# Performance work log

Measured on AMD Instinct MI355X. Metric: run time of the kernel, lower is better.

The kernel has to match this reference:

```python
import jax, jax.numpy as jnp
import numpy as np

N_HEADS = 16

def setup_inputs() -> dict:
    key = jax.random.key(0)
    k1, k2 = jax.random.split(key)
    qkv = jax.random.normal(k1, (4, 3072, 2048), dtype=jnp.float32)
    encoder_kv = jax.random.normal(k2, (4, 2048, 256), dtype=jnp.float32)
    return {"qkv": qkv, "encoder_kv": encoder_kv}

def reference(qkv, encoder_kv):
    bs, width, length = qkv.shape
    ch = width // (3 * N_HEADS)  # 64
    # [bs*H, 3*ch, T] -> q, k, v each [bs*H, ch, T]
    q, k, v = jnp.split(qkv.reshape(bs * N_HEADS, 3 * ch, length), 3, axis=1)
    # encoder kv: [bs, H*2*ch, S] -> ek, ev each [bs*H, ch, S]
    ek, ev = jnp.split(encoder_kv.reshape(bs * N_HEADS, 2 * ch, -1), 2, axis=1)
    k = jnp.concatenate([ek, k], axis=-1)  # [bs*H, ch, S+T]
    v = jnp.concatenate([ev, v], axis=-1)
    scale = ch ** -0.25  # 1/sqrt(sqrt(ch)), applied to both q and k
    weight = jnp.einsum('bct,bcs->bts', q * scale, k * scale)  # [bs*H, T, S+T]
    weight = jax.nn.softmax(weight.astype(jnp.float32), axis=-1).astype(qkv.dtype)
    a = jnp.einsum('bts,bcs->bct', weight, v)  # [bs*H, ch, T]
    return a.reshape(bs, -1, length)
```

## Files before the change

kernel.cpp:

```cpp
#include <hip/hip_runtime.h>
#include <hip/hip_bf16.h>

typedef __attribute__((ext_vector_type(8))) short bf16x8;
typedef __attribute__((ext_vector_type(4))) float f32x4;
typedef __attribute__((ext_vector_type(4))) unsigned u32x4;
typedef __attribute__((ext_vector_type(2))) unsigned u32x2;

#define T_LEN 2048
#define S_ENC 256
#define QSCALE 0.18033688011112042f

#define BARRIER() __syncthreads()

__device__ __forceinline__ float exp2_hw(float x) {
#if __has_builtin(__builtin_amdgcn_exp2f)
  return __builtin_amdgcn_exp2f(x);
#else
  float r;
  asm("v_exp_f32 %0, %1" : "=v"(r) : "v"(x));
  return r;
#endif
}

__device__ __forceinline__ unsigned cvt_pk_bf16(float lo, float hi) {
  unsigned r;
  asm("v_cvt_pk_bf16_f32 %0, %1, %2" : "=v"(r) : "v"(lo), "v"(hi));
  return r;
}

__device__ __forceinline__ short f2bf(float x) {
  union { __hip_bfloat16 b; short s; } u;
  u.b = __float2bfloat16(x);
  return u.s;
}

__device__ __forceinline__ int swz(int row, int col) {
  return row * 64 + (col ^ ((row & 7) << 3));
}

union PU { u32x4 u; bf16x8 b; };

template<int STRIDE>
__device__ __forceinline__ void issue_loads(
    const float* __restrict__ kb, const float* __restrict__ vb, int s0, int tid,
    float (&kr)[8], float (&kr2)[8], f32x4 (&vr)[4]) {
  const int ks = tid & 63;
  const int kc = (tid >> 6) * 8;
  const float* kp = kb + (size_t)kc * STRIDE + (s0 + ks);
  const float* kp2 = kp + (size_t)32 * STRIDE;
#pragma unroll
  for (int r = 0; r < 8; ++r) kr[r] = kp[(size_t)r * STRIDE];
#pragma unroll
  for (int r = 0; r < 8; ++r) kr2[r] = kp2[(size_t)r * STRIDE];
  const int vg = tid & 15;
  const int vc = tid >> 4;
  const float* vp0 = vb + (size_t)vc * STRIDE + (s0 + 4 * vg);
  vr[0] = *(const f32x4*)(vp0);
  vr[1] = *(const f32x4*)(vp0 + (size_t)32 * STRIDE);
  vr[2] = *(const f32x4*)(vp0 + (size_t)16 * STRIDE);
  vr[3] = *(const f32x4*)(vp0 + (size_t)48 * STRIDE);
}

__device__ __forceinline__ void stage_write(
    short* __restrict__ Kt, short* __restrict__ Vt, int tid,
    const float (&kr)[8], const float (&kr2)[8], const f32x4 (&vr)[4]) {
  const int ks = tid & 63;
  const int kc = (tid >> 6) * 8;
  u32x4 kw;
#pragma unroll
  for (int r = 0; r < 4; ++r) kw[r] = cvt_pk_bf16(kr[2 * r], kr[2 * r + 1]);
  *(u32x4*)(Kt + swz(ks, kc)) = kw;
  u32x4 kw2;
#pragma unroll
  for (int r = 0; r < 4; ++r) kw2[r] = cvt_pk_bf16(kr2[2 * r], kr2[2 * r + 1]);
  *(u32x4*)(Kt + swz(ks, kc + 32)) = kw2;

  const int vg = tid & 15;
  const int vc = tid >> 4;
  const int vcol = 32 * (vg >> 3) + 8 * (vg & 3) + 4 * ((vg >> 2) & 1);
  const int vrow[4] = {vc, vc + 32, vc + 16, vc + 48};
#pragma unroll
  for (int i = 0; i < 4; ++i) {
    u32x2 vw;
    vw[0] = cvt_pk_bf16(vr[i][0], vr[i][1]);
    vw[1] = cvt_pk_bf16(vr[i][2], vr[i][3]);
    *(u32x2*)(Vt + swz(vrow[i], vcol)) = vw;
  }
}

__device__ __forceinline__ void compute_tile(
    const short* __restrict__ Kt, const short* __restrict__ Vt,
    const bf16x8 (&qf)[4][2], f32x4 (&o)[4][4], float (&lp)[4], int tid) {
  const int lane = tid & 63;
  const int ln = lane & 15;
  const int lg = lane >> 4;

  bf16x8 kf[4][2];
#pragma unroll
  for (int mt = 0; mt < 4; ++mt) {
    const int row = 16 * mt + ln;
    kf[mt][0] = *(const bf16x8*)(Kt + swz(row, 8 * lg));
    kf[mt][1] = *(const bf16x8*)(Kt + swz(row, 32 + 8 * lg));
  }

  PU pfrag[4][2];
#pragma unroll
  for (int pr = 0; pr < 2; ++pr) {
    f32x4 sacc[2][4];
#pragma unroll
    for (int q2 = 0; q2 < 2; ++q2)
#pragma unroll
      for (int mt = 0; mt < 4; ++mt) sacc[q2][mt] = (f32x4){0.f, 0.f, 0.f, 0.f};

#pragma unroll
    for (int mt = 0; mt < 4; ++mt)
#pragma unroll
      for (int q2 = 0; q2 < 2; ++q2) {
        const int qt = 2 * pr + q2;
        sacc[q2][mt] = __builtin_amdgcn_mfma_f32_16x16x32_bf16(kf[mt][0], qf[qt][0], sacc[q2][mt], 0, 0, 0);
        sacc[q2][mt] = __builtin_amdgcn_mfma_f32_16x16x32_bf16(kf[mt][1], qf[qt][1], sacc[q2][mt], 0, 0, 0);
      }

#pragma unroll
    for (int q2 = 0; q2 < 2; ++q2) {
      const int qt = 2 * pr + q2;
      float pmt[4];
#pragma unroll
      for (int mt = 0; mt < 4; ++mt) {
        float p0 = exp2_hw(sacc[q2][mt][0]);
        float p1 = exp2_hw(sacc[q2][mt][1]);
        float p2 = exp2_hw(sacc[q2][mt][2]);
        float p3 = exp2_hw(sacc[q2][mt][3]);
        pfrag[qt][mt >> 1].u[2 * (mt & 1) + 0] = cvt_pk_bf16(p0, p1);
        pfrag[qt][mt >> 1].u[2 * (mt & 1) + 1] = cvt_pk_bf16(p2, p3);
        pmt[mt] = (p0 + p1) + (p2 + p3);
      }
      lp[qt] += (pmt[0] + pmt[1]) + (pmt[2] + pmt[3]);
    }
  }

#pragma unroll
  for (int sub = 0; sub < 2; ++sub)
#pragma unroll
    for (int ct = 0; ct < 4; ++ct) {
      const bf16x8 vf = *(const bf16x8*)(Vt + swz(16 * ct + ln, 32 * sub + 8 * lg));
#pragma unroll
      for (int qt = 0; qt < 4; ++qt)
        o[qt][ct] = __builtin_amdgcn_mfma_f32_16x16x32_bf16(vf, pfrag[qt][sub].b, o[qt][ct], 0, 0, 0);
    }
}

__global__ __launch_bounds__(256, 2) void attn_kernel(
    const float* __restrict__ qkv, const float* __restrict__ ekv,
    float* __restrict__ out) {
  const int tid = threadIdx.x;
  const int lane = tid & 63;
  const int wave = tid >> 6;
  const int ln = lane & 15;
  const int lg = lane >> 4;

  const int bh = blockIdx.x & 63;
  const int qb = blockIdx.x >> 6;
  const int t0 = qb * 256 + wave * 64;

  const float* qp  = qkv + (size_t)bh * 192 * T_LEN;
  const float* kp  = qp + (size_t)64 * T_LEN;
  const float* vp  = qp + (size_t)128 * T_LEN;
  const float* ekp = ekv + (size_t)bh * 128 * S_ENC;
  const float* evp = ekp + (size_t)64 * S_ENC;

  __shared__ __attribute__((aligned(16))) short Kt[2][64 * 64];
  __shared__ __attribute__((aligned(16))) short Vt[2][64 * 64];

  bf16x8 qf[4][2];
#pragma unroll
  for (int qt = 0; qt < 4; ++qt)
#pragma unroll
    for (int kk = 0; kk < 2; ++kk)
#pragma unroll
      for (int j = 0; j < 8; ++j)
        qf[qt][kk][j] =
            f2bf(qp[(size_t)(32 * kk + 8 * lg + j) * T_LEN + (t0 + 16 * qt + ln)] * QSCALE);

  f32x4 o[4][4];
#pragma unroll
  for (int qt = 0; qt < 4; ++qt)
#pragma unroll
    for (int ct = 0; ct < 4; ++ct) o[qt][ct] = (f32x4){0.f, 0.f, 0.f, 0.f};
  float lp[4] = {0.f, 0.f, 0.f, 0.f};

  for (int st = 0; st < 4; ++st) {
    float kr[8], kr2[8];
    f32x4 vr[4];
    issue_loads<S_ENC>(ekp, evp, 64 * st, tid, kr, kr2, vr);
    BARRIER();
    stage_write(&Kt[0][0], &Vt[0][0], tid, kr, kr2, vr);
    BARRIER();
    compute_tile(&Kt[0][0], &Vt[0][0], qf, o, lp, tid);
  }

  {
    float kr[8], kr2[8];
    f32x4 vr[4];
    issue_loads<T_LEN>(kp, vp, 0, tid, kr, kr2, vr);
    BARRIER();
    stage_write(&Kt[0][0], &Vt[0][0], tid, kr, kr2, vr);
    issue_loads<T_LEN>(kp, vp, 64, tid, kr, kr2, vr);
    BARRIER();

    int cur = 0;
#pragma unroll 1
    for (int t = 0; t < 31; ++t) {
      stage_write(&Kt[cur ^ 1][0], &Vt[cur ^ 1][0], tid, kr, kr2, vr);
      if (t < 30)
        issue_loads<T_LEN>(kp, vp, 64 * (t + 2), tid, kr, kr2, vr);
      compute_tile(&Kt[cur][0], &Vt[cur][0], qf, o, lp, tid);
      BARRIER();
      cur ^= 1;
    }
    compute_tile(&Kt[cur][0], &Vt[cur][0], qf, o, lp, tid);
  }

#pragma unroll
  for (int qt = 0; qt < 4; ++qt) {
    float l = lp[qt];
    l += __shfl_xor(l, 16);
    l += __shfl_xor(l, 32);
    const float inv = 1.0f / l;
    float* ob = out + (size_t)bh * 64 * T_LEN + (t0 + 16 * qt + ln);
#pragma unroll
    for (int ct = 0; ct < 4; ++ct)
#pragma unroll
      for (int r = 0; r < 4; ++r)
        ob[(size_t)(16 * ct + 4 * lg + r) * T_LEN] = o[qt][ct][r] * inv;
  }
}

extern "C" void kernel_launch(void* const* d_in, const int* in_sizes, int n_in,
                              void* d_out, int out_size, void* d_ws, size_t ws_size,
                              hipStream_t stream) {
  const float* qkv = (const float*)d_in[0];
  const float* ekv = (const float*)d_in[1];
  float* out = (float*)d_out;
  attn_kernel<<<dim3(512), dim3(256), 0, stream>>>(qkv, ekv, out);
}
```

Before: 98.77 us.

## Interleave softmax exp with PV MFMAs and drop LDS double buffering

```diff
diff --git a/kernel.cpp b/kernel.cpp
--- a/kernel.cpp
+++ b/kernel.cpp
@@ -9,7 +9,6 @@
 #define T_LEN 2048
 #define S_ENC 256
 #define QSCALE 0.18033688011112042f
-
 #define BARRIER() __syncthreads()
 
 __device__ __forceinline__ float exp2_hw(float x) {
@@ -88,6 +87,22 @@
   }
 }
 
+__device__ __forceinline__ void softmax_qt(const f32x4 (&sa)[4], PU (&pf)[2],
+                                           float& lpq) {
+  float pmt[4];
+#pragma unroll
+  for (int mt = 0; mt < 4; ++mt) {
+    float p0 = exp2_hw(sa[mt][0]);
+    float p1 = exp2_hw(sa[mt][1]);
+    float p2 = exp2_hw(sa[mt][2]);
+    float p3 = exp2_hw(sa[mt][3]);
+    pf[mt >> 1].u[2 * (mt & 1) + 0] = cvt_pk_bf16(p0, p1);
+    pf[mt >> 1].u[2 * (mt & 1) + 1] = cvt_pk_bf16(p2, p3);
+    pmt[mt] = (p0 + p1) + (p2 + p3);
+  }
+  lpq += (pmt[0] + pmt[1]) + (pmt[2] + pmt[3]);
+}
+
 __device__ __forceinline__ void compute_tile(
     const short* __restrict__ Kt, const short* __restrict__ Vt,
     const bf16x8 (&qf)[4][2], f32x4 (&o)[4][4], float (&lp)[4], int tid) {
@@ -103,50 +118,59 @@
     kf[mt][1] = *(const bf16x8*)(Kt + swz(row, 32 + 8 * lg));
   }
 
-  PU pfrag[4][2];
-#pragma unroll
-  for (int pr = 0; pr < 2; ++pr) {
-    f32x4 sacc[2][4];
-#pragma unroll
-    for (int q2 = 0; q2 < 2; ++q2)
-#pragma unroll
-      for (int mt = 0; mt < 4; ++mt) sacc[q2][mt] = (f32x4){0.f, 0.f, 0.f, 0.f};
-
-#pragma unroll
-    for (int mt = 0; mt < 4; ++mt)
-#pragma unroll
-      for (int q2 = 0; q2 < 2; ++q2) {
-        const int qt = 2 * pr + q2;
-        sacc[q2][mt] = __builtin_amdgcn_mfma_f32_16x16x32_bf16(kf[mt][0], qf[qt][0], sacc[q2][mt], 0, 0, 0);
-        sacc[q2][mt] = __builtin_amdgcn_mfma_f32_16x16x32_bf16(kf[mt][1], qf[qt][1], sacc[q2][mt], 0, 0, 0);
-      }
-
+  f32x4 sa[2][4];
+#pragma unroll
+  for (int q2 = 0; q2 < 2; ++q2)
+#pragma unroll
+    for (int mt = 0; mt < 4; ++mt) sa[q2][mt] = (f32x4){0.f, 0.f, 0.f, 0.f};
+#pragma unroll
+  for (int mt = 0; mt < 4; ++mt)
 #pragma unroll
     for (int q2 = 0; q2 < 2; ++q2) {
-      const int qt = 2 * pr + q2;
-      float pmt[4];
-#pragma unroll
-      for (int mt = 0; mt < 4; ++mt) {
-        float p0 = exp2_hw(sacc[q2][mt][0]);
-        float p1 = exp2_hw(sacc[q2][mt][1]);
-        float p2 = exp2_hw(sacc[q2][mt][2]);
-        float p3 = exp2_hw(sacc[q2][mt][3]);
-        pfrag[qt][mt >> 1].u[2 * (mt & 1) + 0] = cvt_pk_bf16(p0, p1);
-        pfrag[qt][mt >> 1].u[2 * (mt & 1) + 1] = cvt_pk_bf16(p2, p3);
-        pmt[mt] = (p0 + p1) + (p2 + p3);
-      }
-      lp[qt] += (pmt[0] + pmt[1]) + (pmt[2] + pmt[3]);
+      sa[q2][mt] = __builtin_amdgcn_mfma_f32_16x16x32_bf16(kf[mt][0], qf[q2][0], sa[q2][mt], 0, 0, 0);
+      sa[q2][mt] = __builtin_amdgcn_mfma_f32_16x16x32_bf16(kf[mt][1], qf[q2][1], sa[q2][mt], 0, 0, 0);
     }
-  }
+
+  PU pf0[2][2];
+  softmax_qt(sa[0], pf0[0], lp[0]);
+  softmax_qt(sa[1], pf0[1], lp[1]);
+
+#pragma unroll
+  for (int q2 = 0; q2 < 2; ++q2)
+#pragma unroll
+    for (int mt = 0; mt < 4; ++mt) sa[q2][mt] = (f32x4){0.f, 0.f, 0.f, 0.f};
+#pragma unroll
+  for (int mt = 0; mt < 4; ++mt)
+#pragma unroll
+    for (int q2 = 0; q2 < 2; ++q2) {
+      sa[q2][mt] = __builtin_amdgcn_mfma_f32_16x16x32_bf16(kf[mt][0], qf[2 + q2][0], sa[q2][mt], 0, 0, 0);
+      sa[q2][mt] = __builtin_amdgcn_mfma_f32_16x16x32_bf16(kf[mt][1], qf[2 + q2][1], sa[q2][mt], 0, 0, 0);
+    }
+
+  bf16x8 vf[2][4];
+  PU pf1[2][2];
+#pragma unroll
+  for (int ct = 0; ct < 4; ++ct) {
+    vf[0][ct] = *(const bf16x8*)(Vt + swz(16 * ct + ln, 8 * lg));
+    o[0][ct] = __builtin_amdgcn_mfma_f32_16x16x32_bf16(vf[0][ct], pf0[0][0].b, o[0][ct], 0, 0, 0);
+    o[1][ct] = __builtin_amdgcn_mfma_f32_16x16x32_bf16(vf[0][ct], pf0[1][0].b, o[1][ct], 0, 0, 0);
+  }
+  softmax_qt(sa[0], pf1[0], lp[2]);
+
+#pragma unroll
+  for (int ct = 0; ct < 4; ++ct) {
+    vf[1][ct] = *(const bf16x8*)(Vt + swz(16 * ct + ln, 32 + 8 * lg));
+    o[0][ct] = __builtin_amdgcn_mfma_f32_16x16x32_bf16(vf[1][ct], pf0[0][1].b, o[0][ct], 0, 0, 0);
+    o[1][ct] = __builtin_amdgcn_mfma_f32_16x16x32_bf16(vf[1][ct], pf0[1][1].b, o[1][ct], 0, 0, 0);
+  }
+  softmax_qt(sa[1], pf1[1], lp[3]);
 
 #pragma unroll
   for (int sub = 0; sub < 2; ++sub)
 #pragma unroll
     for (int ct = 0; ct < 4; ++ct) {
-      const bf16x8 vf = *(const bf16x8*)(Vt + swz(16 * ct + ln, 32 * sub + 8 * lg));
-#pragma unroll
-      for (int qt = 0; qt < 4; ++qt)
-        o[qt][ct] = __builtin_amdgcn_mfma_f32_16x16x32_bf16(vf, pfrag[qt][sub].b, o[qt][ct], 0, 0, 0);
+      o[2][ct] = __builtin_amdgcn_mfma_f32_16x16x32_bf16(vf[sub][ct], pf1[0][sub].b, o[2][ct], 0, 0, 0);
+      o[3][ct] = __builtin_amdgcn_mfma_f32_16x16x32_bf16(vf[sub][ct], pf1[1][sub].b, o[3][ct], 0, 0, 0);
     }
 }
 
@@ -169,8 +193,8 @@
   const float* ekp = ekv + (size_t)bh * 128 * S_ENC;
   const float* evp = ekp + (size_t)64 * S_ENC;
 
-  __shared__ __attribute__((aligned(16))) short Kt[2][64 * 64];
-  __shared__ __attribute__((aligned(16))) short Vt[2][64 * 64];
+  __shared__ __attribute__((aligned(16))) short Kt[64 * 64];
+  __shared__ __attribute__((aligned(16))) short Vt[64 * 64];
 
   bf16x8 qf[4][2];
 #pragma unroll
@@ -194,31 +218,18 @@
     f32x4 vr[4];
     issue_loads<S_ENC>(ekp, evp, 64 * st, tid, kr, kr2, vr);
     BARRIER();
-    stage_write(&Kt[0][0], &Vt[0][0], tid, kr, kr2, vr);
-    BARRIER();
-    compute_tile(&Kt[0][0], &Vt[0][0], qf, o, lp, tid);
-  }
-
-  {
+    stage_write(Kt, Vt, tid, kr, kr2, vr);
+    BARRIER();
+    compute_tile(Kt, Vt, qf, o, lp, tid);
+  }
+  for (int st = 0; st < 32; ++st) {
     float kr[8], kr2[8];
     f32x4 vr[4];
-    issue_loads<T_LEN>(kp, vp, 0, tid, kr, kr2, vr);
-    BARRIER();
-    stage_write(&Kt[0][0], &Vt[0][0], tid, kr, kr2, vr);
-    issue_loads<T_LEN>(kp, vp, 64, tid, kr, kr2, vr);
-    BARRIER();
-
-    int cur = 0;
-#pragma unroll 1
-    for (int t = 0; t < 31; ++t) {
-      stage_write(&Kt[cur ^ 1][0], &Vt[cur ^ 1][0], tid, kr, kr2, vr);
-      if (t < 30)
-        issue_loads<T_LEN>(kp, vp, 64 * (t + 2), tid, kr, kr2, vr);
-      compute_tile(&Kt[cur][0], &Vt[cur][0], qf, o, lp, tid);
-      BARRIER();
-      cur ^= 1;
-    }
-    compute_tile(&Kt[cur][0], &Vt[cur][0], qf, o, lp, tid);
+    issue_loads<T_LEN>(kp, vp, 64 * st, tid, kr, kr2, vr);
+    BARRIER();
+    stage_write(Kt, Vt, tid, kr, kr2, vr);
+    BARRIER();
+    compute_tile(Kt, Vt, qf, o, lp, tid);
   }
 
 #pragma unroll
```

After: 91.78 us. 1.08x faster.

## Load V fragments directly from global memory and drop K double buffering

Applied to the files above, without the earlier changes.

```diff
diff --git a/kernel.cpp b/kernel.cpp
--- a/kernel.cpp
+++ b/kernel.cpp
@@ -4,12 +4,10 @@
 typedef __attribute__((ext_vector_type(8))) short bf16x8;
 typedef __attribute__((ext_vector_type(4))) float f32x4;
 typedef __attribute__((ext_vector_type(4))) unsigned u32x4;
-typedef __attribute__((ext_vector_type(2))) unsigned u32x2;
 
 #define T_LEN 2048
 #define S_ENC 256
 #define QSCALE 0.18033688011112042f
-
 #define BARRIER() __syncthreads()
 
 __device__ __forceinline__ float exp2_hw(float x) {
@@ -42,8 +40,8 @@
 
 template<int STRIDE>
 __device__ __forceinline__ void issue_loads(
-    const float* __restrict__ kb, const float* __restrict__ vb, int s0, int tid,
-    float (&kr)[8], float (&kr2)[8], f32x4 (&vr)[4]) {
+    const float* __restrict__ kb, int s0, int tid,
+    float (&kr)[8], float (&kr2)[8]) {
   const int ks = tid & 63;
   const int kc = (tid >> 6) * 8;
   const float* kp = kb + (size_t)kc * STRIDE + (s0 + ks);
@@ -52,18 +50,11 @@
   for (int r = 0; r < 8; ++r) kr[r] = kp[(size_t)r * STRIDE];
 #pragma unroll
   for (int r = 0; r < 8; ++r) kr2[r] = kp2[(size_t)r * STRIDE];
-  const int vg = tid & 15;
-  const int vc = tid >> 4;
-  const float* vp0 = vb + (size_t)vc * STRIDE + (s0 + 4 * vg);
-  vr[0] = *(const f32x4*)(vp0);
-  vr[1] = *(const f32x4*)(vp0 + (size_t)32 * STRIDE);
-  vr[2] = *(const f32x4*)(vp0 + (size_t)16 * STRIDE);
-  vr[3] = *(const f32x4*)(vp0 + (size_t)48 * STRIDE);
 }
 
 __device__ __forceinline__ void stage_write(
-    short* __restrict__ Kt, short* __restrict__ Vt, int tid,
-    const float (&kr)[8], const float (&kr2)[8], const f32x4 (&vr)[4]) {
+    short* __restrict__ Kt, int tid,
+    const float (&kr)[8], const float (&kr2)[8]) {
   const int ks = tid & 63;
   const int kc = (tid >> 6) * 8;
   u32x4 kw;
@@ -74,26 +65,23 @@
 #pragma unroll
   for (int r = 0; r < 4; ++r) kw2[r] = cvt_pk_bf16(kr2[2 * r], kr2[2 * r + 1]);
   *(u32x4*)(Kt + swz(ks, kc + 32)) = kw2;
-
-  const int vg = tid & 15;
-  const int vc = tid >> 4;
-  const int vcol = 32 * (vg >> 3) + 8 * (vg & 3) + 4 * ((vg >> 2) & 1);
-  const int vrow[4] = {vc, vc + 32, vc + 16, vc + 48};
-#pragma unroll
-  for (int i = 0; i < 4; ++i) {
-    u32x2 vw;
-    vw[0] = cvt_pk_bf16(vr[i][0], vr[i][1]);
-    vw[1] = cvt_pk_bf16(vr[i][2], vr[i][3]);
-    *(u32x2*)(Vt + swz(vrow[i], vcol)) = vw;
-  }
-}
-
+}
+
+template<int STRIDE>
 __device__ __forceinline__ void compute_tile(
-    const short* __restrict__ Kt, const short* __restrict__ Vt,
+    const short* __restrict__ Kt, const float* __restrict__ vt ,
     const bf16x8 (&qf)[4][2], f32x4 (&o)[4][4], float (&lp)[4], int tid) {
   const int lane = tid & 63;
   const int ln = lane & 15;
   const int lg = lane >> 4;
+
+  f32x4 va[4], vb_[4], vc_[4], vd[4];
+#pragma unroll
+  for (int ct = 0; ct < 4; ++ct) {
+    const float* p = vt + (size_t)(16 * ct + ln) * STRIDE + 4 * lg;
+    va[ct] = *(const f32x4*)p;
+    vb_[ct] = *(const f32x4*)(p + 16);
+  }
 
   bf16x8 kf[4][2];
 #pragma unroll
@@ -120,6 +108,15 @@
         sacc[q2][mt] = __builtin_amdgcn_mfma_f32_16x16x32_bf16(kf[mt][0], qf[qt][0], sacc[q2][mt], 0, 0, 0);
         sacc[q2][mt] = __builtin_amdgcn_mfma_f32_16x16x32_bf16(kf[mt][1], qf[qt][1], sacc[q2][mt], 0, 0, 0);
       }
+
+    if (pr == 0) {
+#pragma unroll
+      for (int ct = 0; ct < 4; ++ct) {
+        const float* p = vt + (size_t)(16 * ct + ln) * STRIDE + 32 + 4 * lg;
+        vc_[ct] = *(const f32x4*)p;
+        vd[ct] = *(const f32x4*)(p + 16);
+      }
+    }
 
 #pragma unroll
     for (int q2 = 0; q2 < 2; ++q2) {
@@ -143,10 +140,16 @@
   for (int sub = 0; sub < 2; ++sub)
 #pragma unroll
     for (int ct = 0; ct < 4; ++ct) {
-      const bf16x8 vf = *(const bf16x8*)(Vt + swz(16 * ct + ln, 32 * sub + 8 * lg));
+      const f32x4 lo = sub ? vc_[ct] : va[ct];
+      const f32x4 hi = sub ? vd[ct] : vb_[ct];
+      PU vf;
+      vf.u[0] = cvt_pk_bf16(lo[0], lo[1]);
+      vf.u[1] = cvt_pk_bf16(lo[2], lo[3]);
+      vf.u[2] = cvt_pk_bf16(hi[0], hi[1]);
+      vf.u[3] = cvt_pk_bf16(hi[2], hi[3]);
 #pragma unroll
       for (int qt = 0; qt < 4; ++qt)
-        o[qt][ct] = __builtin_amdgcn_mfma_f32_16x16x32_bf16(vf, pfrag[qt][sub].b, o[qt][ct], 0, 0, 0);
+        o[qt][ct] = __builtin_amdgcn_mfma_f32_16x16x32_bf16(vf.b, pfrag[qt][sub].b, o[qt][ct], 0, 0, 0);
     }
 }
 
@@ -169,8 +172,7 @@
   const float* ekp = ekv + (size_t)bh * 128 * S_ENC;
   const float* evp = ekp + (size_t)64 * S_ENC;
 
-  __shared__ __attribute__((aligned(16))) short Kt[2][64 * 64];
-  __shared__ __attribute__((aligned(16))) short Vt[2][64 * 64];
+  __shared__ __attribute__((aligned(16))) short Kt[64 * 64];
 
   bf16x8 qf[4][2];
 #pragma unroll
@@ -191,34 +193,19 @@
 
   for (int st = 0; st < 4; ++st) {
     float kr[8], kr2[8];
-    f32x4 vr[4];
-    issue_loads<S_ENC>(ekp, evp, 64 * st, tid, kr, kr2, vr);
-    BARRIER();
-    stage_write(&Kt[0][0], &Vt[0][0], tid, kr, kr2, vr);
-    BARRIER();
-    compute_tile(&Kt[0][0], &Vt[0][0], qf, o, lp, tid);
-  }
-
-  {
+    issue_loads<S_ENC>(ekp, 64 * st, tid, kr, kr2);
+    BARRIER();
+    stage_write(Kt, tid, kr, kr2);
+    BARRIER();
+    compute_tile<S_ENC>(Kt, evp + 64 * st, qf, o, lp, tid);
+  }
+  for (int st = 0; st < 32; ++st) {
     float kr[8], kr2[8];
-    f32x4 vr[4];
-    issue_loads<T_LEN>(kp, vp, 0, tid, kr, kr2, vr);
-    BARRIER();
-    stage_write(&Kt[0][0], &Vt[0][0], tid, kr, kr2, vr);
-    issue_loads<T_LEN>(kp, vp, 64, tid, kr, kr2, vr);
-    BARRIER();
-
-    int cur = 0;
-#pragma unroll 1
-    for (int t = 0; t < 31; ++t) {
-      stage_write(&Kt[cur ^ 1][0], &Vt[cur ^ 1][0], tid, kr, kr2, vr);
-      if (t < 30)
-        issue_loads<T_LEN>(kp, vp, 64 * (t + 2), tid, kr, kr2, vr);
-      compute_tile(&Kt[cur][0], &Vt[cur][0], qf, o, lp, tid);
-      BARRIER();
-      cur ^= 1;
-    }
-    compute_tile(&Kt[cur][0], &Vt[cur][0], qf, o, lp, tid);
+    issue_loads<T_LEN>(kp, 64 * st, tid, kr, kr2);
+    BARRIER();
+    stage_write(Kt, tid, kr, kr2);
+    BARRIER();
+    compute_tile<T_LEN>(Kt, vp + 64 * st, qf, o, lp, tid);
   }
 
 #pragma unroll
```

Result: slower. 197.9 us (+100.4%).

## Replace software-pipelined K/V loop with batched two-tile load-then-compute and MFMA priority

Applied to the files above, without the earlier changes.

```diff
diff --git a/kernel.cpp b/kernel.cpp
--- a/kernel.cpp
+++ b/kernel.cpp
@@ -9,7 +9,6 @@
 #define T_LEN 2048
 #define S_ENC 256
 #define QSCALE 0.18033688011112042f
-
 #define BARRIER() __syncthreads()
 
 __device__ __forceinline__ float exp2_hw(float x) {
@@ -112,6 +111,7 @@
 #pragma unroll
       for (int mt = 0; mt < 4; ++mt) sacc[q2][mt] = (f32x4){0.f, 0.f, 0.f, 0.f};
 
+    __builtin_amdgcn_s_setprio(1);
 #pragma unroll
     for (int mt = 0; mt < 4; ++mt)
 #pragma unroll
@@ -120,6 +120,7 @@
         sacc[q2][mt] = __builtin_amdgcn_mfma_f32_16x16x32_bf16(kf[mt][0], qf[qt][0], sacc[q2][mt], 0, 0, 0);
         sacc[q2][mt] = __builtin_amdgcn_mfma_f32_16x16x32_bf16(kf[mt][1], qf[qt][1], sacc[q2][mt], 0, 0, 0);
       }
+    __builtin_amdgcn_s_setprio(0);
 
 #pragma unroll
     for (int q2 = 0; q2 < 2; ++q2) {
@@ -139,6 +140,7 @@
     }
   }
 
+  __builtin_amdgcn_s_setprio(1);
 #pragma unroll
   for (int sub = 0; sub < 2; ++sub)
 #pragma unroll
@@ -148,6 +150,7 @@
       for (int qt = 0; qt < 4; ++qt)
         o[qt][ct] = __builtin_amdgcn_mfma_f32_16x16x32_bf16(vf, pfrag[qt][sub].b, o[qt][ct], 0, 0, 0);
     }
+  __builtin_amdgcn_s_setprio(0);
 }
 
 __global__ __launch_bounds__(256, 2) void attn_kernel(
@@ -189,36 +192,29 @@
     for (int ct = 0; ct < 4; ++ct) o[qt][ct] = (f32x4){0.f, 0.f, 0.f, 0.f};
   float lp[4] = {0.f, 0.f, 0.f, 0.f};
 
-  for (int st = 0; st < 4; ++st) {
-    float kr[8], kr2[8];
-    f32x4 vr[4];
-    issue_loads<S_ENC>(ekp, evp, 64 * st, tid, kr, kr2, vr);
-    BARRIER();
-    stage_write(&Kt[0][0], &Vt[0][0], tid, kr, kr2, vr);
+  for (int st = 0; st < 2; ++st) {
+    float krA[8], kr2A[8], krB[8], kr2B[8];
+    f32x4 vrA[4], vrB[4];
+    issue_loads<S_ENC>(ekp, evp, 128 * st, tid, krA, kr2A, vrA);
+    issue_loads<S_ENC>(ekp, evp, 128 * st + 64, tid, krB, kr2B, vrB);
+    BARRIER();
+    stage_write(&Kt[0][0], &Vt[0][0], tid, krA, kr2A, vrA);
+    stage_write(&Kt[1][0], &Vt[1][0], tid, krB, kr2B, vrB);
     BARRIER();
     compute_tile(&Kt[0][0], &Vt[0][0], qf, o, lp, tid);
-  }
-
-  {
-    float kr[8], kr2[8];
-    f32x4 vr[4];
-    issue_loads<T_LEN>(kp, vp, 0, tid, kr, kr2, vr);
-    BARRIER();
-    stage_write(&Kt[0][0], &Vt[0][0], tid, kr, kr2, vr);
-    issue_loads<T_LEN>(kp, vp, 64, tid, kr, kr2, vr);
-    BARRIER();
-
-    int cur = 0;
-#pragma unroll 1
-    for (int t = 0; t < 31; ++t) {
-      stage_write(&Kt[cur ^ 1][0], &Vt[cur ^ 1][0], tid, kr, kr2, vr);
-      if (t < 30)
-        issue_loads<T_LEN>(kp, vp, 64 * (t + 2), tid, kr, kr2, vr);
-      compute_tile(&Kt[cur][0], &Vt[cur][0], qf, o, lp, tid);
-      BARRIER();
-      cur ^= 1;
-    }
-    compute_tile(&Kt[cur][0], &Vt[cur][0], qf, o, lp, tid);
+    compute_tile(&Kt[1][0], &Vt[1][0], qf, o, lp, tid);
+  }
+  for (int st = 0; st < 16; ++st) {
+    float krA[8], kr2A[8], krB[8], kr2B[8];
+    f32x4 vrA[4], vrB[4];
+    issue_loads<T_LEN>(kp, vp, 128 * st, tid, krA, kr2A, vrA);
+    issue_loads<T_LEN>(kp, vp, 128 * st + 64, tid, krB, kr2B, vrB);
+    BARRIER();
+    stage_write(&Kt[0][0], &Vt[0][0], tid, krA, kr2A, vrA);
+    stage_write(&Kt[1][0], &Vt[1][0], tid, krB, kr2B, vrB);
+    BARRIER();
+    compute_tile(&Kt[0][0], &Vt[0][0], qf, o, lp, tid);
+    compute_tile(&Kt[1][0], &Vt[1][0], qf, o, lp, tid);
   }
 
 #pragma unroll
```

After: 93.22 us. 1.06x faster.
